# Kernel optimization log

Measured on AMD Instinct MI355X. Metric: run time of the kernel, lower is better.

## Reference

```python
import jax, jax.numpy as jnp
import numpy as np

B, N, S, K, NDIM, HID = 2, 8192, 1024, 32, 3, 256


def _sincos_embed(pos, dim):
    # pos: (..., ndim) continuous coordinates -> (..., dim) sincos embedding
    ndim = pos.shape[-1]
    emb_dim_per_dim = dim // ndim
    half = emb_dim_per_dim // 2
    freq = jnp.exp(jnp.arange(half, dtype=pos.dtype) * (-np.log(10000.0) / (half - 1)))
    embs = []
    for i in range(ndim):
        e = pos[..., i:i + 1] * freq  # (..., half)
        embs.append(jnp.concatenate([jnp.sin(e), jnp.cos(e)], axis=-1))
    x = jnp.concatenate(embs, axis=-1)  # (..., ndim*2*half)
    pad = dim - x.shape[-1]
    if pad > 0:
        x = jnp.pad(x, [(0, 0)] * (x.ndim - 1) + [(0, pad)])
    return x


def setup_inputs() -> dict:
    key = jax.random.key(0)
    ks = jax.random.split(key, 8)
    input_pos = jax.random.normal(ks[0], (B, N, NDIM), dtype=jnp.float32)
    supernode_idxs = jax.random.randint(ks[1], (S,), 0, N)
    # lecun_normal-style init (stddev = 1/sqrt(fan_in)), zero bias (torch/flax Dense default bias=0)
    w_in = jax.random.normal(ks[2], (NDIM, HID), dtype=jnp.float32) / np.sqrt(NDIM)
    b_in = jnp.zeros((HID,), jnp.float32)
    w1 = jax.random.normal(ks[3], (HID, HID), dtype=jnp.float32) / np.sqrt(HID)
    b1 = jnp.zeros((HID,), jnp.float32)
    w2 = jax.random.normal(ks[4], (HID, HID), dtype=jnp.float32) / np.sqrt(HID)
    b2 = jnp.zeros((HID,), jnp.float32)
    return {"input_pos": input_pos, "supernode_idxs": supernode_idxs,
            "w_in": w_in, "b_in": b_in, "w1": w1, "b1": b1, "w2": w2, "b2": b2}


def reference(input_pos, supernode_idxs, w_in, b_in, w1, b1, w2, b2):
    def knn(x):  # x: (N, ndim)
        # Euclidean distance from each supernode to every point: (S, N).
        # Same values as rows of the full NxN cdist the original materializes.
        d = jnp.sqrt(jnp.sum((x[supernode_idxs][:, None, :] - x[None, :, :]) ** 2, axis=-1))
        nbr = jnp.argsort(d, axis=1)[:, :K]  # (S, K)
        return x[nbr]  # (S, K, ndim)

    coords = jax.vmap(knn)(input_pos)  # (B, S, K, ndim)
    proj = coords @ w_in + b_in                         # (B, S, K, HID)
    pe = _sincos_embed(coords, HID)                     # (B, S, K, HID)
    h = proj + pe
    h = jax.nn.gelu(h @ w1 + b1) @ w2 + b2              # message MLP
    return jnp.mean(h, axis=-2)                         # (B, S, HID)
```

## Files before the change

kernel.cpp:

```cpp
#include <hip/hip_runtime.h>
#include <hip/hip_bf16.h>
#include <math.h>

#define BB   2
#define NN   8192
#define SS   1024
#define KK   32
#define HID  256
#define SENT 0xFFFFFFFFFFFFFFFFULL
#define LDB  264
#define WFE  65536

typedef unsigned long long u64;
typedef unsigned int       u32;
typedef short bf16x8 __attribute__((ext_vector_type(8)));
typedef float f32x4  __attribute__((ext_vector_type(4)));

#define CSW(SI) { const u64 mn = x < (SI) ? x : (SI); const u64 mx = x < (SI) ? (SI) : x; (SI) = mn; x = mx; }
#define INS5(KV) { u64 x = (KV); CSW(s0) CSW(s1) CSW(s2) CSW(s3) CSW(s4) }
#define INS3HI(KV) { u64 x = (KV); CSW(s5) CSW(s6) CSW(s7) }
#define INS8(KV) { u64 x = (KV); CSW(s0) CSW(s1) CSW(s2) CSW(s3) CSW(s4) CSW(s5) CSW(s6) CSW(s7) }

#define DIST_KEY(i, kv)                                                        \
    const float dx = __fsub_rn(sx, posb[(i)*3 + 0]);                           \
    const float dy = __fsub_rn(sy, posb[(i)*3 + 1]);                           \
    const float dz = __fsub_rn(sz, posb[(i)*3 + 2]);                           \
    const float sq = __fadd_rn(__fadd_rn(__fmul_rn(dx,dx), __fmul_rn(dy,dy)),  \
                               __fmul_rn(dz,dz));                              \
    const u64 kv = ((u64)__float_as_uint(__fsqrt_rn(sq)) << 13) | (u32)(i);

__device__ __forceinline__ float tanh_fast(float y) {
    const float e = __expf(2.0f * y);
    const float r = __builtin_amdgcn_rcpf(e + 1.0f);
    return fmaf(-2.0f, r, 1.0f);
}

__device__ __forceinline__ short bf_bits(float f) {
    const __hip_bfloat16 h = __float2bfloat16(f);
    short s;
    __builtin_memcpy(&s, &h, 2);
    return s;
}

__device__ __forceinline__ int mbcnt64(u64 m) {
    return (int)__builtin_amdgcn_mbcnt_hi((u32)(m >> 32),
           __builtin_amdgcn_mbcnt_lo((u32)m, 0u));
}

__global__ void prep_w(const float* __restrict__ w1, const float* __restrict__ w2,
                       __hip_bfloat16* __restrict__ wf) {
    const int idx = blockIdx.x * 256 + threadIdx.x;
    const int j   = idx & 7;
    const int l   = (idx >> 3) & 63;
    const int ntg = (idx >> 9) & 15;
    const int ks  = (idx >> 13) & 7;
    const int mat = idx >> 16;
    const int k = ks * 32 + (l >> 4) * 8 + j;
    const int n = ntg * 16 + (l & 15);
    const float v = (mat ? w2 : w1)[k * HID + n];
    const __hip_bfloat16 hi = __float2bfloat16(v);
    const float res = v - __bfloat162float(hi);
    const size_t s0 = (size_t)mat * 131072 + ((size_t)((ks*16 + ntg)*2) * 64 + l) * 8 + j;
    wf[s0]       = hi;
    wf[s0 + 512] = __float2bfloat16(res);
}

__global__ __launch_bounds__(256, 8)
void knn_kernel(const float* __restrict__ pos,
                const int*   __restrict__ snidx,
                int*         __restrict__ nbr_g)
{
    const int bs   = blockIdx.x;
    const int b    = bs / SS;
    const int s    = bs - b * SS;
    const int t    = threadIdx.x;
    const int lane = t & 63;
    const int wv   = t >> 6;

    __shared__ u64 wl[4 * KK];

    const float* posb = pos + (size_t)b * (NN * 3);
    const int   sp = snidx[s];
    const float sx = posb[sp*3 + 0];
    const float sy = posb[sp*3 + 1];
    const float sz = posb[sp*3 + 2];

    u64 s0=SENT,s1=SENT,s2=SENT,s3=SENT,s4=SENT,s5=SENT,s6=SENT,s7=SENT;
#pragma unroll 4
    for (int c = 0; c < 32; ++c) {
        const int i = c * 256 + t;
        DIST_KEY(i, kv)
        INS5(kv);
    }

#define CNT5(CAND) (__popcll(__ballot(s0<(CAND)))+__popcll(__ballot(s1<(CAND))) \
                   +__popcll(__ballot(s2<(CAND)))+__popcll(__ballot(s3<(CAND))) \
                   +__popcll(__ballot(s4<(CAND))))
#define CNT8(CAND) (CNT5(CAND)+__popcll(__ballot(s5<(CAND))) \
                   +__popcll(__ballot(s6<(CAND)))+__popcll(__ballot(s7<(CAND))))

    {
        u64 L = 0;
        for (int bit = 43; bit >= 13; --bit) {
            const u64 cand = L | (1ull << bit);
            if (CNT5(cand) < 32) L = cand;
        }
        u64 TH = L + (1ull << 13);
        if (CNT5(TH) != 32) {
            for (int bit = 12; bit >= 0; --bit) {
                const u64 cand = L | (1ull << bit);
                if (CNT5(cand) < 32) L = cand;
            }
            TH = L + 1;
        }
        bool b0 = s0 < TH, b1 = s1 < TH, b2 = s2 < TH, b3 = s3 < TH, b4 = s4 < TH;
        bool b5 = false, b6 = false, b7 = false;
        const int csel5 = (int)b0+(int)b1+(int)b2+(int)b3+(int)b4;
        bool need_serial = false;

        if (__ballot(csel5 == 5) != 0ull) {
            s5 = s6 = s7 = SENT;
#pragma unroll 4
            for (int c = 0; c < 32; ++c) {
                const int i = c * 256 + t;
                DIST_KEY(i, kv)
                const u64 kf = kv > s4 ? kv : SENT;
                INS3HI(kf);
            }
            u64 L8 = 0;
            for (int bit = 43; bit >= 13; --bit) {
                const u64 cand = L8 | (1ull << bit);
                if (CNT8(cand) < 32) L8 = cand;
            }
            u64 TH8 = L8 + (1ull << 13);
            if (CNT8(TH8) != 32) {
                for (int bit = 12; bit >= 0; --bit) {
                    const u64 cand = L8 | (1ull << bit);
                    if (CNT8(cand) < 32) L8 = cand;
                }
                TH8 = L8 + 1;
            }
            b0 = s0 < TH8; b1 = s1 < TH8; b2 = s2 < TH8; b3 = s3 < TH8;
            b4 = s4 < TH8; b5 = s5 < TH8; b6 = s6 < TH8; b7 = s7 < TH8;
            const int csel8 = (int)b0+(int)b1+(int)b2+(int)b3
                            + (int)b4+(int)b5+(int)b6+(int)b7;
            need_serial = __ballot(csel8 == 8) != 0ull;
        }

        if (need_serial) {
            int nv = (int)(s0!=SENT)+(int)(s1!=SENT)+(int)(s2!=SENT)+(int)(s3!=SENT)
                   + (int)(s4!=SENT)+(int)(s5!=SENT)+(int)(s6!=SENT)+(int)(s7!=SENT);
#pragma unroll 1
            for (int it = 0; it < KK; ++it) {
                u64 m = s0;
#pragma unroll
                for (int off = 32; off > 0; off >>= 1) {
                    const u64 o = __shfl_xor(m, off, 64);
                    m = o < m ? o : m;
                }
                if (lane == 0) wl[wv*KK + it] = m;
                if (s0 == m) {
                    s0=s1; s1=s2; s2=s3; s3=s4; s4=s5; s5=s6; s6=s7; s7=SENT;
                    if (--nv == 0) {
                        const u64 last = m;
                        s0=s1=s2=s3=s4=s5=s6=s7=SENT;
#pragma unroll 4
                        for (int c = 0; c < 32; ++c) {
                            const int i = c * 256 + t;
                            DIST_KEY(i, kv)
                            const u64 kf = kv > last ? kv : SENT;
                            INS8(kf);
                        }
                        nv = (int)(s0!=SENT)+(int)(s1!=SENT)+(int)(s2!=SENT)+(int)(s3!=SENT)
                           + (int)(s4!=SENT)+(int)(s5!=SENT)+(int)(s6!=SENT)+(int)(s7!=SENT);
                    }
                }
            }
        } else {
            const u64 m0=__ballot(b0), m1=__ballot(b1), m2=__ballot(b2), m3=__ballot(b3),
                      m4=__ballot(b4), m5=__ballot(b5), m6=__ballot(b6), m7=__ballot(b7);
            int p = mbcnt64(m0)+mbcnt64(m1)+mbcnt64(m2)+mbcnt64(m3)
                  + mbcnt64(m4)+mbcnt64(m5)+mbcnt64(m6)+mbcnt64(m7);
            u64* wwl = &wl[wv * KK];
            if (b0) { wwl[p] = s0; ++p; }
            if (b1) { wwl[p] = s1; ++p; }
            if (b2) { wwl[p] = s2; ++p; }
            if (b3) { wwl[p] = s3; ++p; }
            if (b4) { wwl[p] = s4; ++p; }
            if (b5) { wwl[p] = s5; ++p; }
            if (b6) { wwl[p] = s6; ++p; }
            if (b7) { wwl[p] = s7; }
        }
    }
    __syncthreads();

    if (t < 64) {
        const u64 k0 = wl[lane], k1 = wl[64 + lane];
        u64 L = 0;
        for (int bit = 43; bit >= 13; --bit) {
            const u64 cand = L | (1ull << bit);
            const int cnt = __popcll(__ballot(k0 < cand)) + __popcll(__ballot(k1 < cand));
            if (cnt < 32) L = cand;
        }
        u64 TH = L + (1ull << 13);
        {
            const int cnt = __popcll(__ballot(k0 < TH)) + __popcll(__ballot(k1 < TH));
            if (cnt != 32) {
                for (int bit = 12; bit >= 0; --bit) {
                    const u64 cand = L | (1ull << bit);
                    const int c2 = __popcll(__ballot(k0 < cand)) + __popcll(__ballot(k1 < cand));
                    if (c2 < 32) L = cand;
                }
                TH = L + 1;
            }
        }
        const bool c0 = k0 < TH, c1 = k1 < TH;
        const int p = mbcnt64(__ballot(c0)) + mbcnt64(__ballot(c1));
        if (c0) nbr_g[(size_t)bs * KK + p]           = (int)(k0 & 8191u);
        if (c1) nbr_g[(size_t)bs * KK + p + (int)c0] = (int)(k1 & 8191u);
    }
}

__global__ __launch_bounds__(256, 4)
void mlp_kernel(const float* __restrict__ pos,
                const int*   __restrict__ nbr_g,
                const float* __restrict__ w_in,
                const float* __restrict__ b_in,
                const float* __restrict__ b1,
                const float* __restrict__ b2,
                const __hip_bfloat16* __restrict__ wf,
                float*       __restrict__ out)
{
    const int tk0  = blockIdx.x * 2;
    const int b    = tk0 / SS;
    const int t    = threadIdx.x;
    const int lane = t & 63;
    const int wv   = t >> 6;

    __shared__ __align__(16) short h0b[2 * KK][LDB];
    __shared__ __align__(16) float nbc[2 * 4 * KK];

    const float* posb = pos + (size_t)b * (NN * 3);

    if (t < 2 * KK * 3) {
        const int k = t / 3, d = t - 3 * k;
        nbc[k * 4 + d] = posb[(size_t)nbr_g[(size_t)tk0 * KK + k] * 3 + d];
    }
    __syncthreads();

    {
        const int  c     = t;
        const int  dimi  = c / 84;
        const int  cc    = c - dimi * 84;
        const bool hasPe = c < 252;
        const bool isCos = cc >= 42;
        const int  f     = isCos ? cc - 42 : cc;
        const float fcoef = (float)(-9.210340371976184 / 41.0);
        const float freqv = expf((float)f * fcoef);
        const int  di    = hasPe ? dimi : 0;

        const float wi0 = w_in[0*HID + c];
        const float wi1 = w_in[1*HID + c];
        const float wi2 = w_in[2*HID + c];
        const float bi  = b_in[c];

#pragma unroll 4
        for (int k = 0; k < 2 * KK; ++k) {
            const float4 xv4 = *(const float4*)&nbc[k * 4];
            const float x0 = xv4.x, x1 = xv4.y, x2 = xv4.z;
            float v = fmaf(x2, wi2, fmaf(x1, wi1, fmaf(x0, wi0, bi)));
            if (hasPe) {
                const float xv  = (di == 0) ? x0 : ((di == 1) ? x1 : x2);
                const float ang = xv * freqv;
                v += isCos ? __cosf(ang) : __sinf(ang);
            }
            h0b[k][c] = bf_bits(v);
        }
    }
    __syncthreads();

    const int lr = lane & 15;
    const int lg = lane >> 4;
    const int nbase = wv * 64;

    const short* arow0 = &h0b[lr][lg * 8];
    const short* arow1 = &h0b[16 + lr][lg * 8];
    const short* arow2 = &h0b[32 + lr][lg * 8];
    const short* arow3 = &h0b[48 + lr][lg * 8];
    const __hip_bfloat16* wb1 = wf + (size_t)wv * 4096 + lane * 8;
    const __hip_bfloat16* wb2 = wb1 + 2 * WFE;

    f32x4 acc[4][4];

    {
#pragma unroll
        for (int nt = 0; nt < 4; ++nt) {
            const float bias = b1[nbase + nt*16 + lr];
            const f32x4 bv = {bias, bias, bias, bias};
            acc[0][nt] = bv; acc[1][nt] = bv; acc[2][nt] = bv; acc[3][nt] = bv;
        }
#pragma unroll 1
        for (int ks = 0; ks < 8; ++ks) {
            const bf16x8 af0 = *(const bf16x8*)(arow0 + ks * 32);
            const bf16x8 af1 = *(const bf16x8*)(arow1 + ks * 32);
            const bf16x8 af2 = *(const bf16x8*)(arow2 + ks * 32);
            const bf16x8 af3 = *(const bf16x8*)(arow3 + ks * 32);
            const __hip_bfloat16* p = wb1 + ks * 16384;
#pragma unroll
            for (int nt = 0; nt < 4; ++nt) {
                const bf16x8 bh = *(const bf16x8*)(p + nt * 1024);
                acc[0][nt] = __builtin_amdgcn_mfma_f32_16x16x32_bf16(af0, bh, acc[0][nt], 0,0,0);
                acc[1][nt] = __builtin_amdgcn_mfma_f32_16x16x32_bf16(af1, bh, acc[1][nt], 0,0,0);
                acc[2][nt] = __builtin_amdgcn_mfma_f32_16x16x32_bf16(af2, bh, acc[2][nt], 0,0,0);
                acc[3][nt] = __builtin_amdgcn_mfma_f32_16x16x32_bf16(af3, bh, acc[3][nt], 0,0,0);
                const bf16x8 bl = *(const bf16x8*)(p + nt * 1024 + 512);
                acc[0][nt] = __builtin_amdgcn_mfma_f32_16x16x32_bf16(af0, bl, acc[0][nt], 0,0,0);
                acc[1][nt] = __builtin_amdgcn_mfma_f32_16x16x32_bf16(af1, bl, acc[1][nt], 0,0,0);
                acc[2][nt] = __builtin_amdgcn_mfma_f32_16x16x32_bf16(af2, bl, acc[2][nt], 0,0,0);
                acc[3][nt] = __builtin_amdgcn_mfma_f32_16x16x32_bf16(af3, bl, acc[3][nt], 0,0,0);
            }
        }
    }
    __syncthreads();

    {
        const float kA = 0.7978845608028654f;
#pragma unroll
        for (int mt = 0; mt < 4; ++mt)
#pragma unroll
        for (int nt = 0; nt < 4; ++nt)
#pragma unroll
        for (int r = 0; r < 4; ++r) {
            const float x  = acc[mt][nt][r];
            const float x3 = x * x * x;
            const float tv = tanh_fast(kA * fmaf(0.044715f, x3, x));
            h0b[mt*16 + lg*4 + r][nbase + nt*16 + lr] = bf_bits(0.5f * x * (1.0f + tv));
        }
    }
    __syncthreads();

    {
        const f32x4 z = {0.f, 0.f, 0.f, 0.f};
#pragma unroll
        for (int nt = 0; nt < 4; ++nt) {
            acc[0][nt] = z; acc[1][nt] = z; acc[2][nt] = z; acc[3][nt] = z;
        }
#pragma unroll 1
        for (int ks = 0; ks < 8; ++ks) {
            const bf16x8 af0 = *(const bf16x8*)(arow0 + ks * 32);
            const bf16x8 af1 = *(const bf16x8*)(arow1 + ks * 32);
            const bf16x8 af2 = *(const bf16x8*)(arow2 + ks * 32);
            const bf16x8 af3 = *(const bf16x8*)(arow3 + ks * 32);
            const __hip_bfloat16* p = wb2 + ks * 16384;
#pragma unroll
            for (int nt = 0; nt < 4; ++nt) {
                const bf16x8 bh = *(const bf16x8*)(p + nt * 1024);
                acc[0][nt] = __builtin_amdgcn_mfma_f32_16x16x32_bf16(af0, bh, acc[0][nt], 0,0,0);
                acc[1][nt] = __builtin_amdgcn_mfma_f32_16x16x32_bf16(af1, bh, acc[1][nt], 0,0,0);
                acc[2][nt] = __builtin_amdgcn_mfma_f32_16x16x32_bf16(af2, bh, acc[2][nt], 0,0,0);
                acc[3][nt] = __builtin_amdgcn_mfma_f32_16x16x32_bf16(af3, bh, acc[3][nt], 0,0,0);
                const bf16x8 bl = *(const bf16x8*)(p + nt * 1024 + 512);
                acc[0][nt] = __builtin_amdgcn_mfma_f32_16x16x32_bf16(af0, bl, acc[0][nt], 0,0,0);
                acc[1][nt] = __builtin_amdgcn_mfma_f32_16x16x32_bf16(af1, bl, acc[1][nt], 0,0,0);
                acc[2][nt] = __builtin_amdgcn_mfma_f32_16x16x32_bf16(af2, bl, acc[2][nt], 0,0,0);
                acc[3][nt] = __builtin_amdgcn_mfma_f32_16x16x32_bf16(af3, bl, acc[3][nt], 0,0,0);
            }
        }
    }

#pragma unroll
    for (int nt = 0; nt < 4; ++nt) {
        float sumA = 0.0f, sumB = 0.0f;
#pragma unroll
        for (int r = 0; r < 4; ++r) {
            sumA += acc[0][nt][r] + acc[1][nt][r];
            sumB += acc[2][nt][r] + acc[3][nt][r];
        }
        sumA += __shfl_xor(sumA, 16, 64); sumA += __shfl_xor(sumA, 32, 64);
        sumB += __shfl_xor(sumB, 16, 64); sumB += __shfl_xor(sumB, 32, 64);
        if (lane < 16) {
            const int ch = wv * 64 + nt*16 + lane;
            const float bb = b2[ch];
            out[(size_t)tk0 * HID + ch]       = fmaf(sumA, 1.0f / KK, bb);
            out[(size_t)(tk0 + 1) * HID + ch] = fmaf(sumB, 1.0f / KK, bb);
        }
    }
}

extern "C" void kernel_launch(void* const* d_in, const int* in_sizes, int n_in,
                              void* d_out, int out_size, void* d_ws, size_t ws_size,
                              hipStream_t stream) {
    const float* pos  = (const float*)d_in[0];
    const int*   sni  = (const int*)  d_in[1];
    const float* w_in = (const float*)d_in[2];
    const float* b_in = (const float*)d_in[3];
    const float* w1   = (const float*)d_in[4];
    const float* b1   = (const float*)d_in[5];
    const float* w2   = (const float*)d_in[6];
    const float* b2   = (const float*)d_in[7];
    float* out = (float*)d_out;
    __hip_bfloat16* wf = (__hip_bfloat16*)d_ws;
    int* nbr_g = (int*)((char*)d_ws + 4 * WFE * 2);
    (void)ws_size; (void)in_sizes; (void)n_in; (void)out_size;

    hipLaunchKernelGGL(prep_w, dim3(2 * WFE / 256), dim3(256), 0, stream, w1, w2, wf);
    hipLaunchKernelGGL(knn_kernel, dim3(BB * SS), dim3(256), 0, stream, pos, sni, nbr_g);
    hipLaunchKernelGGL(mlp_kernel, dim3(BB * SS / 2), dim3(256), 0, stream,
                       pos, nbr_g, w_in, b_in, b1, b2, wf, out);
}
```

Baseline: 78.45 us.

## Fold weight prep into kNN launch and compute input embedding there

Removes the separate weight-prep launch by giving those blocks a leading range of the kNN grid. After selecting neighbours, each kNN block now gathers coordinates and computes the input projection plus sincos embedding in bf16. It writes them to a global workspace, and a slimmer MLP kernel only loads them and runs the two GEMMs. This adds about 33 MB of global traffic and a workspace-size dependence, with the old fused MLP kept as a fallback.

```diff
diff --git a/kernel.cpp b/kernel.cpp
--- a/kernel.cpp
+++ b/kernel.cpp
@@ -10,6 +10,7 @@
 #define SENT 0xFFFFFFFFFFFFFFFFULL
 #define LDB  264
 #define WFE  65536
+#define PREPB 512
 
 typedef unsigned long long u64;
 typedef unsigned int       u32;
@@ -47,37 +48,45 @@
            __builtin_amdgcn_mbcnt_lo((u32)m, 0u));
 }
 
-__global__ void prep_w(const float* __restrict__ w1, const float* __restrict__ w2,
-                       __hip_bfloat16* __restrict__ wf) {
-    const int idx = blockIdx.x * 256 + threadIdx.x;
-    const int j   = idx & 7;
-    const int l   = (idx >> 3) & 63;
-    const int ntg = (idx >> 9) & 15;
-    const int ks  = (idx >> 13) & 7;
-    const int mat = idx >> 16;
-    const int k = ks * 32 + (l >> 4) * 8 + j;
-    const int n = ntg * 16 + (l & 15);
-    const float v = (mat ? w2 : w1)[k * HID + n];
-    const __hip_bfloat16 hi = __float2bfloat16(v);
-    const float res = v - __bfloat162float(hi);
-    const size_t s0 = (size_t)mat * 131072 + ((size_t)((ks*16 + ntg)*2) * 64 + l) * 8 + j;
-    wf[s0]       = hi;
-    wf[s0 + 512] = __float2bfloat16(res);
-}
-
 __global__ __launch_bounds__(256, 8)
 void knn_kernel(const float* __restrict__ pos,
                 const int*   __restrict__ snidx,
-                int*         __restrict__ nbr_g)
+                const float* __restrict__ w1,
+                const float* __restrict__ w2,
+                __hip_bfloat16* __restrict__ wf,
+                int*         __restrict__ nbr_g,
+                const float* __restrict__ w_in,
+                const float* __restrict__ b_in,
+                short*       __restrict__ h0g)
 {
-    const int bs   = blockIdx.x;
+    if (blockIdx.x < PREPB) {
+        const int idx = blockIdx.x * 256 + threadIdx.x;
+        const int j   = idx & 7;
+        const int l   = (idx >> 3) & 63;
+        const int ntg = (idx >> 9) & 15;
+        const int ks  = (idx >> 13) & 7;
+        const int mat = idx >> 16;
+        const int k = ks * 32 + (l >> 4) * 8 + j;
+        const int n = ntg * 16 + (l & 15);
+        const float v = (mat ? w2 : w1)[k * HID + n];
+        const __hip_bfloat16 hi = __float2bfloat16(v);
+        const float res = v - __bfloat162float(hi);
+        const size_t sl = (size_t)mat * 131072 + ((size_t)((ks*16 + ntg)*2) * 64 + l) * 8 + j;
+        wf[sl]       = hi;
+        wf[sl + 512] = __float2bfloat16(res);
+        return;
+    }
+
+    const int bs   = blockIdx.x - PREPB;
     const int b    = bs / SS;
     const int s    = bs - b * SS;
     const int t    = threadIdx.x;
     const int lane = t & 63;
     const int wv   = t >> 6;
 
-    __shared__ u64 wl[4 * KK];
+    __shared__ u64   wl[4 * KK];
+    __shared__ int   nbrl[KK];
+    __shared__ __align__(16) float nbc[4 * KK];
 
     const float* posb = pos + (size_t)b * (NN * 3);
     const int   sp = snidx[s];
@@ -216,20 +225,196 @@
         }
         const bool c0 = k0 < TH, c1 = k1 < TH;
         const int p = mbcnt64(__ballot(c0)) + mbcnt64(__ballot(c1));
-        if (c0) nbr_g[(size_t)bs * KK + p]           = (int)(k0 & 8191u);
-        if (c1) nbr_g[(size_t)bs * KK + p + (int)c0] = (int)(k1 & 8191u);
+        if (c0) { nbrl[p] = (int)(k0 & 8191u);
+                  nbr_g[(size_t)bs * KK + p] = nbrl[p]; }
+        if (c1) { nbrl[p + (int)c0] = (int)(k1 & 8191u);
+                  nbr_g[(size_t)bs * KK + p + (int)c0] = nbrl[p + (int)c0]; }
+    }
+
+    if (h0g == nullptr) return;
+    __syncthreads();
+
+    if (t < KK * 3) {
+        const int k = t / 3, d = t - 3 * k;
+        nbc[k * 4 + d] = posb[(size_t)nbrl[k] * 3 + d];
+    }
+    __syncthreads();
+
+    {
+        const int  c     = t;
+        const int  dimi  = c / 84;
+        const int  cc    = c - dimi * 84;
+        const bool hasPe = c < 252;
+        const bool isCos = cc >= 42;
+        const int  f     = isCos ? cc - 42 : cc;
+        const float fcoef = (float)(-9.210340371976184 / 41.0);
+        const float freqv = expf((float)f * fcoef);
+        const int  di    = hasPe ? dimi : 0;
+
+        const float wi0 = w_in[0*HID + c];
+        const float wi1 = w_in[1*HID + c];
+        const float wi2 = w_in[2*HID + c];
+        const float bi  = b_in[c];
+
+        short* dst = h0g + (size_t)bs * KK * HID + c;
+#pragma unroll 4
+        for (int k = 0; k < KK; ++k) {
+            const float4 xv4 = *(const float4*)&nbc[k * 4];
+            const float x0 = xv4.x, x1 = xv4.y, x2 = xv4.z;
+            float v = fmaf(x2, wi2, fmaf(x1, wi1, fmaf(x0, wi0, bi)));
+            if (hasPe) {
+                const float xv  = (di == 0) ? x0 : ((di == 1) ? x1 : x2);
+                const float ang = xv * freqv;
+                v += isCos ? __cosf(ang) : __sinf(ang);
+            }
+            dst[k * HID] = bf_bits(v);
+        }
     }
 }
 
 __global__ __launch_bounds__(256, 4)
-void mlp_kernel(const float* __restrict__ pos,
-                const int*   __restrict__ nbr_g,
-                const float* __restrict__ w_in,
-                const float* __restrict__ b_in,
-                const float* __restrict__ b1,
-                const float* __restrict__ b2,
-                const __hip_bfloat16* __restrict__ wf,
-                float*       __restrict__ out)
+void mlp_split(const short* __restrict__ h0g,
+               const float* __restrict__ b1,
+               const float* __restrict__ b2,
+               const __hip_bfloat16* __restrict__ wf,
+               float*       __restrict__ out)
+{
+    const int tk0  = blockIdx.x * 2;
+    const int t    = threadIdx.x;
+    const int lane = t & 63;
+    const int wv   = t >> 6;
+
+    __shared__ __align__(16) short h0b[2 * KK][LDB];
+
+    {
+        const short* src = h0g + (size_t)tk0 * KK * HID;
+#pragma unroll
+        for (int it = 0; it < 8; ++it) {
+            const int e   = it * 256 + t;
+            const int row = e >> 5;
+            const int col = (e & 31) * 8;
+            *(bf16x8*)&h0b[row][col] = *(const bf16x8*)(src + (size_t)e * 8);
+        }
+    }
+    __syncthreads();
+
+    const int lr = lane & 15;
+    const int lg = lane >> 4;
+    const int nbase = wv * 64;
+
+    const short* arow0 = &h0b[lr][lg * 8];
+    const short* arow1 = &h0b[16 + lr][lg * 8];
+    const short* arow2 = &h0b[32 + lr][lg * 8];
+    const short* arow3 = &h0b[48 + lr][lg * 8];
+    const __hip_bfloat16* wb1 = wf + (size_t)wv * 4096 + lane * 8;
+    const __hip_bfloat16* wb2 = wb1 + 2 * WFE;
+
+    f32x4 acc[4][4];
+
+    {
+#pragma unroll
+        for (int nt = 0; nt < 4; ++nt) {
+            const float bias = b1[nbase + nt*16 + lr];
+            const f32x4 bv = {bias, bias, bias, bias};
+            acc[0][nt] = bv; acc[1][nt] = bv; acc[2][nt] = bv; acc[3][nt] = bv;
+        }
+#pragma unroll 1
+        for (int ks = 0; ks < 8; ++ks) {
+            const bf16x8 af0 = *(const bf16x8*)(arow0 + ks * 32);
+            const bf16x8 af1 = *(const bf16x8*)(arow1 + ks * 32);
+            const bf16x8 af2 = *(const bf16x8*)(arow2 + ks * 32);
+            const bf16x8 af3 = *(const bf16x8*)(arow3 + ks * 32);
+            const __hip_bfloat16* p = wb1 + ks * 16384;
+#pragma unroll
+            for (int nt = 0; nt < 4; ++nt) {
+                const bf16x8 bh = *(const bf16x8*)(p + nt * 1024);
+                acc[0][nt] = __builtin_amdgcn_mfma_f32_16x16x32_bf16(af0, bh, acc[0][nt], 0,0,0);
+                acc[1][nt] = __builtin_amdgcn_mfma_f32_16x16x32_bf16(af1, bh, acc[1][nt], 0,0,0);
+                acc[2][nt] = __builtin_amdgcn_mfma_f32_16x16x32_bf16(af2, bh, acc[2][nt], 0,0,0);
+                acc[3][nt] = __builtin_amdgcn_mfma_f32_16x16x32_bf16(af3, bh, acc[3][nt], 0,0,0);
+                const bf16x8 bl = *(const bf16x8*)(p + nt * 1024 + 512);
+                acc[0][nt] = __builtin_amdgcn_mfma_f32_16x16x32_bf16(af0, bl, acc[0][nt], 0,0,0);
+                acc[1][nt] = __builtin_amdgcn_mfma_f32_16x16x32_bf16(af1, bl, acc[1][nt], 0,0,0);
+                acc[2][nt] = __builtin_amdgcn_mfma_f32_16x16x32_bf16(af2, bl, acc[2][nt], 0,0,0);
+                acc[3][nt] = __builtin_amdgcn_mfma_f32_16x16x32_bf16(af3, bl, acc[3][nt], 0,0,0);
+            }
+        }
+    }
+    __syncthreads();
+
+    {
+        const float kA = 0.7978845608028654f;
+#pragma unroll
+        for (int mt = 0; mt < 4; ++mt)
+#pragma unroll
+        for (int nt = 0; nt < 4; ++nt)
+#pragma unroll
+        for (int r = 0; r < 4; ++r) {
+            const float x  = acc[mt][nt][r];
+            const float x3 = x * x * x;
+            const float tv = tanh_fast(kA * fmaf(0.044715f, x3, x));
+            h0b[mt*16 + lg*4 + r][nbase + nt*16 + lr] = bf_bits(0.5f * x * (1.0f + tv));
+        }
+    }
+    __syncthreads();
+
+    {
+        const f32x4 z = {0.f, 0.f, 0.f, 0.f};
+#pragma unroll
+        for (int nt = 0; nt < 4; ++nt) {
+            acc[0][nt] = z; acc[1][nt] = z; acc[2][nt] = z; acc[3][nt] = z;
+        }
+#pragma unroll 1
+        for (int ks = 0; ks < 8; ++ks) {
+            const bf16x8 af0 = *(const bf16x8*)(arow0 + ks * 32);
+            const bf16x8 af1 = *(const bf16x8*)(arow1 + ks * 32);
+            const bf16x8 af2 = *(const bf16x8*)(arow2 + ks * 32);
+            const bf16x8 af3 = *(const bf16x8*)(arow3 + ks * 32);
+            const __hip_bfloat16* p = wb2 + ks * 16384;
+#pragma unroll
+            for (int nt = 0; nt < 4; ++nt) {
+                const bf16x8 bh = *(const bf16x8*)(p + nt * 1024);
+                acc[0][nt] = __builtin_amdgcn_mfma_f32_16x16x32_bf16(af0, bh, acc[0][nt], 0,0,0);
+                acc[1][nt] = __builtin_amdgcn_mfma_f32_16x16x32_bf16(af1, bh, acc[1][nt], 0,0,0);
+                acc[2][nt] = __builtin_amdgcn_mfma_f32_16x16x32_bf16(af2, bh, acc[2][nt], 0,0,0);
+                acc[3][nt] = __builtin_amdgcn_mfma_f32_16x16x32_bf16(af3, bh, acc[3][nt], 0,0,0);
+                const bf16x8 bl = *(const bf16x8*)(p + nt * 1024 + 512);
+                acc[0][nt] = __builtin_amdgcn_mfma_f32_16x16x32_bf16(af0, bl, acc[0][nt], 0,0,0);
+                acc[1][nt] = __builtin_amdgcn_mfma_f32_16x16x32_bf16(af1, bl, acc[1][nt], 0,0,0);
+                acc[2][nt] = __builtin_amdgcn_mfma_f32_16x16x32_bf16(af2, bl, acc[2][nt], 0,0,0);
+                acc[3][nt] = __builtin_amdgcn_mfma_f32_16x16x32_bf16(af3, bl, acc[3][nt], 0,0,0);
+            }
+        }
+    }
+
+#pragma unroll
+    for (int nt = 0; nt < 4; ++nt) {
+        float sumA = 0.0f, sumB = 0.0f;
+#pragma unroll
+        for (int r = 0; r < 4; ++r) {
+            sumA += acc[0][nt][r] + acc[1][nt][r];
+            sumB += acc[2][nt][r] + acc[3][nt][r];
+        }
+        sumA += __shfl_xor(sumA, 16, 64); sumA += __shfl_xor(sumA, 32, 64);
+        sumB += __shfl_xor(sumB, 16, 64); sumB += __shfl_xor(sumB, 32, 64);
+        if (lane < 16) {
+            const int ch = wv * 64 + nt*16 + lane;
+            const float bb = b2[ch];
+            out[(size_t)tk0 * HID + ch]       = fmaf(sumA, 1.0f / KK, bb);
+            out[(size_t)(tk0 + 1) * HID + ch] = fmaf(sumB, 1.0f / KK, bb);
+        }
+    }
+}
+
+__global__ __launch_bounds__(256, 4)
+void mlp_fb(const float* __restrict__ pos,
+            const int*   __restrict__ nbr_g,
+            const float* __restrict__ w_in,
+            const float* __restrict__ b_in,
+            const float* __restrict__ b1,
+            const float* __restrict__ b2,
+            const __hip_bfloat16* __restrict__ wf,
+            float*       __restrict__ out)
 {
     const int tk0  = blockIdx.x * 2;
     const int b    = tk0 / SS;
@@ -401,10 +586,20 @@
     float* out = (float*)d_out;
     __hip_bfloat16* wf = (__hip_bfloat16*)d_ws;
     int* nbr_g = (int*)((char*)d_ws + 4 * WFE * 2);
-    (void)ws_size; (void)in_sizes; (void)n_in; (void)out_size;
-
-    hipLaunchKernelGGL(prep_w, dim3(2 * WFE / 256), dim3(256), 0, stream, w1, w2, wf);
-    hipLaunchKernelGGL(knn_kernel, dim3(BB * SS), dim3(256), 0, stream, pos, sni, nbr_g);
-    hipLaunchKernelGGL(mlp_kernel, dim3(BB * SS / 2), dim3(256), 0, stream,
-                       pos, nbr_g, w_in, b_in, b1, b2, wf, out);
+    short* h0g = (short*)((char*)d_ws + 4 * WFE * 2 + (size_t)BB*SS*KK*4);
+    const size_t need = 4*(size_t)WFE*2 + (size_t)BB*SS*KK*4
+                      + (size_t)BB*SS*KK*HID*2;
+    const bool split = ws_size >= need;
+    (void)in_sizes; (void)n_in; (void)out_size;
+
+    hipLaunchKernelGGL(knn_kernel, dim3(PREPB + BB * SS), dim3(256), 0, stream,
+                       pos, sni, w1, w2, wf, nbr_g, w_in, b_in,
+                       split ? h0g : (short*)nullptr);
+    if (split) {
+        hipLaunchKernelGGL(mlp_split, dim3(BB * SS / 2), dim3(256), 0, stream,
+                           h0g, b1, b2, wf, out);
+    } else {
+        hipLaunchKernelGGL(mlp_fb, dim3(BB * SS / 2), dim3(256), 0, stream,
+                           pos, nbr_g, w_in, b_in, b1, b2, wf, out);
+    }
 }
```

After: 84.26 us. 1.07x slower.
